# Performance work log

Hardware: AMD Instinct MI355X
Metric: run time of the kernel (lower is better)

The kernel has to match this reference:

```python
import jax, jax.numpy as jnp
import numpy as np

B, S, D = 1, 2048, 4096
H, KVH, HD = 32, 8, 128
ROPE_THETA = 10000.0


def setup_inputs() -> dict:
    key = jax.random.key(0)
    k1, k2, k3, k4, k5 = jax.random.split(key, 5)
    scale = D ** -0.5
    return {
        "hidden_states": jax.random.normal(k1, (B, S, D), dtype=jnp.float32),
        "position_ids": jnp.arange(S, dtype=jnp.int64).reshape(1, S),
        "Wq": jax.random.normal(k2, (H * HD, D), dtype=jnp.float32) * scale,
        "Wk": jax.random.normal(k3, (KVH * HD, D), dtype=jnp.float32) * scale,
        "Wv": jax.random.normal(k4, (KVH * HD, D), dtype=jnp.float32) * scale,
        "Wo": jax.random.normal(k5, (D, H * HD), dtype=jnp.float32) * scale,
    }


def _rotate_half(x):
    x1, x2 = x[..., : HD // 2], x[..., HD // 2 :]
    return jnp.concatenate((-x2, x1), axis=-1)


def reference(hidden_states, position_ids, Wq, Wk, Wv, Wo):
    b, s, d = hidden_states.shape
    # projections: nn.Linear applies x @ W.T
    q = jnp.einsum("bsd,ed->bse", hidden_states, Wq).reshape(b, s, H, HD).transpose(0, 2, 1, 3)
    k = jnp.einsum("bsd,ed->bse", hidden_states, Wk).reshape(b, s, KVH, HD).transpose(0, 2, 1, 3)
    v = jnp.einsum("bsd,ed->bse", hidden_states, Wv).reshape(b, s, KVH, HD).transpose(0, 2, 1, 3)
    # rotary embedding (default rope: inv_freq = theta^(-2i/d), attention_scaling = 1)
    inv_freq = 1.0 / (ROPE_THETA ** (jnp.arange(0, HD, 2, dtype=jnp.float32) / HD))
    pos = position_ids.astype(jnp.float32)  # [Bp, S]
    freqs = pos[:, :, None] * inv_freq[None, None, :]  # [Bp, S, HD/2]
    emb = jnp.concatenate((freqs, freqs), axis=-1)  # [Bp, S, HD]
    cos = jnp.cos(emb)[:, None, :, :]  # unsqueeze head dim
    sin = jnp.sin(emb)[:, None, :, :]
    q = q * cos + _rotate_half(q) * sin
    k = k * cos + _rotate_half(k) * sin
    # GQA: expand kv heads to match query heads
    groups = H // KVH
    k = jnp.repeat(k, groups, axis=1)
    v = jnp.repeat(v, groups, axis=1)
    # causal attention, scaling = head_dim^-0.5
    scores = jnp.einsum("bhqd,bhkd->bhqk", q, k) * (HD ** -0.5)
    causal = jnp.tril(jnp.ones((s, s), dtype=bool))
    scores = jnp.where(causal[None, None], scores, jnp.finfo(scores.dtype).min)
    attn = jax.nn.softmax(scores, axis=-1)
    out = jnp.einsum("bhqk,bhkd->bhqd", attn, v)
    out = out.transpose(0, 2, 1, 3).reshape(b, s, H * HD)
    return jnp.einsum("bse,de->bsd", out, Wo)
```

## Files before the change

### kernel.cpp

```cpp
#include <hip/hip_runtime.h>
#include <stdint.h>

typedef unsigned short u16;
typedef __attribute__((ext_vector_type(4))) float f32x4;
typedef __attribute__((ext_vector_type(8))) short bf16x8;

static constexpr int S   = 2048;
static constexpr int DM  = 4096;
static constexpr int NH  = 32;
static constexpr int NKV = 8;
static constexpr int HD  = 128;
static constexpr int LDQ = 5120;

__device__ __forceinline__ u16 f2bf(float f) {
    union { float f; unsigned u; } v; v.f = f;
    return (u16)((v.u + 0x7FFFu + ((v.u >> 16) & 1u)) >> 16);
}
__device__ __forceinline__ float bf2f(u16 h) {
    union { unsigned u; float f; } v; v.u = ((unsigned)h) << 16;
    return v.f;
}
__device__ __forceinline__ unsigned pk2bf(float lo, float hi) {
    unsigned r;
    asm("v_cvt_pk_bf16_f32 %0, %1, %2" : "=v"(r) : "v"(lo), "v"(hi));
    return r;
}

__device__ __forceinline__ void mfma16(f32x4& d, bf16x8 a, bf16x8 b) {
    asm("v_mfma_f32_16x16x32_bf16 %0, %1, %2, %0" : "+v"(d) : "v"(a), "v"(b));
}

__device__ __forceinline__ void gload_lds16(const u16* g, u16* lds) {
    __builtin_amdgcn_global_load_lds((__attribute__((address_space(1))) void*)g,
                                     (__attribute__((address_space(3))) void*)lds,
                                     16, 0, 0);
}

__global__ __launch_bounds__(256) void cvt_all(const float* __restrict__ X,
                                               const float* __restrict__ Wq,
                                               const float* __restrict__ Wk,
                                               const float* __restrict__ Wv,
                                               const float* __restrict__ Wo,
                                               u16* __restrict__ out) {
    const int n4 = 12582912;
    int i = blockIdx.x * blockDim.x + threadIdx.x;
    int stride = gridDim.x * blockDim.x;
    for (; i < n4; i += stride) {
        float4 v;
        if (i < 2097152)       v = ((const float4*)X)[i];
        else if (i < 6291456)  v = ((const float4*)Wq)[i - 2097152];
        else if (i < 7340032)  v = ((const float4*)Wk)[i - 6291456];
        else if (i < 8388608)  v = ((const float4*)Wv)[i - 7340032];
        else                   v = ((const float4*)Wo)[i - 8388608];
        ushort4 o;
        o.x = f2bf(v.x); o.y = f2bf(v.y); o.z = f2bf(v.z); o.w = f2bf(v.w);
        ((ushort4*)out)[i] = o;
    }
}

__global__ __launch_bounds__(256) void rope_table_kernel(float2* __restrict__ tbl) {
    int i = blockIdx.x * blockDim.x + threadIdx.x;
    if (i >= S * 64) return;
    int p = i >> 6, j = i & 63;
    float inv = powf(10000.0f, -(float)j / 64.0f);
    float a = (float)p * inv;
    tbl[i] = make_float2(cosf(a), sinf(a));
}

__global__ __launch_bounds__(256) void rope2_kernel(u16* __restrict__ X,
                                                    const float2* __restrict__ tbl,
                                                    float qscale) {
    int i = blockIdx.x * blockDim.x + threadIdx.x;
    const int total = S * 40 * 64;
    if (i >= total) return;
    int dd = i & 63;
    int t2 = i >> 6;
    int hh = t2 % 40;
    int s  = t2 / 40;
    size_t base;
    float scale;
    if (hh < 32) { base = (size_t)s * LDQ + hh * HD + dd;               scale = qscale; }
    else         { base = (size_t)s * LDQ + 4096 + (hh - 32) * HD + dd; scale = 1.0f;   }
    float x1 = bf2f(X[base]);
    float x2 = bf2f(X[base + 64]);
    float2 cs = tbl[(s << 6) + dd];
    X[base]      = f2bf((x1 * cs.x - x2 * cs.y) * scale);
    X[base + 64] = f2bf((x2 * cs.x + x1 * cs.y) * scale);
}

__global__ __launch_bounds__(256)
void gemm_bt(const u16* __restrict__ A, const u16* __restrict__ Bt,
             float* __restrict__ C, int M, int N, int K, int lda, int ldb, int ldc) {
    __shared__ u16 Al[128 * 64];
    __shared__ u16 Bl[128 * 64];
    const int t = threadIdx.x;
    const int w = t >> 6, l = t & 63;
    const int r16 = l & 15, g4 = l >> 4;
    const int m0 = blockIdx.y * 128, n0 = blockIdx.x * 128;
    const int wr = (w >> 1) * 64, wc = (w & 1) * 64;

    f32x4 acc[4][4];
#pragma unroll
    for (int i = 0; i < 4; ++i)
#pragma unroll
        for (int j = 0; j < 4; ++j) acc[i][j] = f32x4{0.f, 0.f, 0.f, 0.f};

    for (int kt = 0; kt < K; kt += 64) {
#pragma unroll
        for (int i = 0; i < 4; ++i) {
            int c = i * 256 + t;
            int r = c >> 3, s = (c & 7) ^ (r & 7);
            gload_lds16(A + (size_t)(m0 + r) * lda + kt + (s << 3),
                        Al + ((i * 256 + w * 64) << 3));
        }
#pragma unroll
        for (int i = 0; i < 4; ++i) {
            int c = i * 256 + t;
            int r = c >> 3, s = (c & 7) ^ (r & 7);
            gload_lds16(Bt + (size_t)(n0 + r) * ldb + kt + (s << 3),
                        Bl + ((i * 256 + w * 64) << 3));
        }
        asm volatile("s_waitcnt vmcnt(0)" ::: "memory");
        __syncthreads();

#pragma unroll
        for (int kk = 0; kk < 2; ++kk) {
            bf16x8 af[4], bfr[4];
#pragma unroll
            for (int mi = 0; mi < 4; ++mi) {
                int r = wr + mi * 16 + r16;
                af[mi] = *(const bf16x8*)((const char*)Al +
                          ((r * 128 + kk * 64 + g4 * 16) ^ ((r & 7) << 4)));
            }
#pragma unroll
            for (int ni = 0; ni < 4; ++ni) {
                int r = wc + ni * 16 + r16;
                bfr[ni] = *(const bf16x8*)((const char*)Bl +
                           ((r * 128 + kk * 64 + g4 * 16) ^ ((r & 7) << 4)));
            }
#pragma unroll
            for (int mi = 0; mi < 4; ++mi)
#pragma unroll
                for (int ni = 0; ni < 4; ++ni)
                    mfma16(acc[mi][ni], af[mi], bfr[ni]);
        }
        __syncthreads();
    }

    const int rb = g4 * 4;
#pragma unroll
    for (int mi = 0; mi < 4; ++mi)
#pragma unroll
        for (int ni = 0; ni < 4; ++ni) {
            const int n = n0 + wc + ni * 16 + r16;
            const int mbase = m0 + wr + mi * 16 + rb;
#pragma unroll
            for (int j = 0; j < 4; ++j)
                C[(size_t)(mbase + j) * ldc + n] = acc[mi][ni][j];
        }
}

__global__ __launch_bounds__(256)
void gemm_qkv(const u16* __restrict__ A, const u16* __restrict__ Bt,
              u16* __restrict__ Cqk, u16* __restrict__ Vt) {
    __shared__ u16 Al[128 * 64];
    __shared__ u16 Bl[128 * 64];
    const int t = threadIdx.x;
    const int w = t >> 6, l = t & 63;
    const int r16 = l & 15, g4 = l >> 4;
    const int m0 = blockIdx.y * 128, n0 = blockIdx.x * 128;
    const int wr = (w >> 1) * 64, wc = (w & 1) * 64;

    f32x4 acc[4][4];
#pragma unroll
    for (int i = 0; i < 4; ++i)
#pragma unroll
        for (int j = 0; j < 4; ++j) acc[i][j] = f32x4{0.f, 0.f, 0.f, 0.f};

    for (int kt = 0; kt < DM; kt += 64) {
#pragma unroll
        for (int i = 0; i < 4; ++i) {
            int c = i * 256 + t;
            int r = c >> 3, s = (c & 7) ^ (r & 7);
            gload_lds16(A + (size_t)(m0 + r) * DM + kt + (s << 3),
                        Al + ((i * 256 + w * 64) << 3));
        }
#pragma unroll
        for (int i = 0; i < 4; ++i) {
            int c = i * 256 + t;
            int r = c >> 3, s = (c & 7) ^ (r & 7);
            gload_lds16(Bt + (size_t)(n0 + r) * DM + kt + (s << 3),
                        Bl + ((i * 256 + w * 64) << 3));
        }
        asm volatile("s_waitcnt vmcnt(0)" ::: "memory");
        __syncthreads();

#pragma unroll
        for (int kk = 0; kk < 2; ++kk) {
            bf16x8 af[4], bfr[4];
#pragma unroll
            for (int mi = 0; mi < 4; ++mi) {
                int r = wr + mi * 16 + r16;
                af[mi] = *(const bf16x8*)((const char*)Al +
                          ((r * 128 + kk * 64 + g4 * 16) ^ ((r & 7) << 4)));
            }
#pragma unroll
            for (int ni = 0; ni < 4; ++ni) {
                int r = wc + ni * 16 + r16;
                bfr[ni] = *(const bf16x8*)((const char*)Bl +
                           ((r * 128 + kk * 64 + g4 * 16) ^ ((r & 7) << 4)));
            }
#pragma unroll
            for (int mi = 0; mi < 4; ++mi)
#pragma unroll
                for (int ni = 0; ni < 4; ++ni)
                    mfma16(acc[mi][ni], af[mi], bfr[ni]);
        }
        __syncthreads();
    }

    const int rb = g4 * 4;
    if (n0 < 5120) {
#pragma unroll
        for (int mi = 0; mi < 4; ++mi)
#pragma unroll
            for (int ni = 0; ni < 4; ++ni) {
                const int n = n0 + wc + ni * 16 + r16;
                const int mbase = m0 + wr + mi * 16 + rb;
#pragma unroll
                for (int j = 0; j < 4; ++j)
                    Cqk[(size_t)(mbase + j) * LDQ + n] = f2bf(acc[mi][ni][j]);
            }
    } else {
#pragma unroll
        for (int mi = 0; mi < 4; ++mi)
#pragma unroll
            for (int ni = 0; ni < 4; ++ni) {
                const int n = n0 + wc + ni * 16 + r16 - 5120;
                const int mbase = m0 + wr + mi * 16 + rb;
                ushort4 v4;
                v4.x = f2bf(acc[mi][ni][0]); v4.y = f2bf(acc[mi][ni][1]);
                v4.z = f2bf(acc[mi][ni][2]); v4.w = f2bf(acc[mi][ni][3]);
                *(ushort4*)&Vt[(size_t)n * S + mbase] = v4;
            }
    }
}

__global__ __launch_bounds__(256, 2)
void attn_fwd(const u16* __restrict__ QK, const u16* __restrict__ Vt,
              u16* __restrict__ O) {
    __shared__ u16 Kl[2][64 * 128];
    __shared__ u16 Vl[2][128 * 64];
    __shared__ u16 Pl[4 * 1024];

    const int t = threadIdx.x;
    const int w = t >> 6, l = t & 63;
    const int r16 = l & 15, g4 = l >> 4;
    const int h = blockIdx.y;
    const int kvh = h >> 2;
    const int p = blockIdx.x;
    const int q0A = p * 64, q0B = (31 - p) * 64;
    const int ntA = p + 1, ntB = 32 - p;

    const u16* Kg = QK + 4096 + kvh * HD;
    const u16* Vg = Vt + (size_t)(kvh * HD) * S;
    u16* Pb = &Pl[w * 1024];

    bf16x8 qfA[4], qfB[4];
    {
        const u16* Qg = QK + h * HD;
        const size_t qrA = (size_t)(q0A + w * 16 + r16) * LDQ;
        const size_t qrB = (size_t)(q0B + w * 16 + r16) * LDQ;
#pragma unroll
        for (int kg = 0; kg < 4; ++kg) {
            qfA[kg] = *(const bf16x8*)&Qg[qrA + kg * 32 + g4 * 8];
            qfB[kg] = *(const bf16x8*)&Qg[qrB + kg * 32 + g4 * 8];
        }
    }

    f32x4 accA[8], accB[8];
    float mA = -3.0e38f, lA = 0.f, mB = -3.0e38f, lB = 0.f;
#pragma unroll
    for (int i = 0; i < 8; ++i) { accA[i] = f32x4{0,0,0,0}; accB[i] = f32x4{0,0,0,0}; }

    auto stage = [&](int tk, int b) {
        const int kv0 = tk * 64;
#pragma unroll
        for (int i = 0; i < 4; ++i) {
            int c = i * 256 + t;
            int r = c >> 4, s = (c & 15) ^ (r & 7);
            gload_lds16(Kg + (size_t)(kv0 + r) * LDQ + (s << 3),
                        &Kl[b][0] + ((i * 256 + w * 64) << 3));
        }
#pragma unroll
        for (int i = 0; i < 4; ++i) {
            int c = i * 256 + t;
            int r = c >> 3, s = (c & 7) ^ (r & 7);
            gload_lds16(Vg + (size_t)r * S + kv0 + (s << 3),
                        &Vl[b][0] + ((i * 256 + w * 64) << 3));
        }
    };

    auto compute = [&](f32x4 (&acco)[8], float& mrun, float& lrun,
                       const bf16x8 (&qf)[4], int q0, int tk, bool maskit, int b) {
        const int kv0 = tk * 64;
        const u16* Kb = &Kl[b][0];
        const u16* Vb = &Vl[b][0];

        f32x4 sc[4];
#pragma unroll
        for (int ni = 0; ni < 4; ++ni) sc[ni] = f32x4{0,0,0,0};
        __builtin_amdgcn_s_setprio(1);
#pragma unroll
        for (int kg = 0; kg < 4; ++kg) {
#pragma unroll
            for (int ni = 0; ni < 4; ++ni) {
                int row = ni * 16 + r16;
                int bb = (row * 256 + kg * 64 + g4 * 16) ^ ((row & 7) << 4);
                bf16x8 kf = *(const bf16x8*)((const char*)Kb + bb);
                mfma16(sc[ni], kf, qf[kg]);
            }
        }
        __builtin_amdgcn_s_setprio(0);

        const int qg = q0 + (w << 4) + r16;
        if (maskit) {
#pragma unroll
            for (int ni = 0; ni < 4; ++ni)
#pragma unroll
                for (int j = 0; j < 4; ++j)
                    if (kv0 + ni * 16 + g4 * 4 + j > qg) sc[ni][j] = -3.0e38f;
        }

        float v = fmaxf(fmaxf(fmaxf(sc[0][0], sc[0][1]), fmaxf(sc[0][2], sc[0][3])),
                        fmaxf(fmaxf(sc[1][0], sc[1][1]), fmaxf(sc[1][2], sc[1][3])));
        v = fmaxf(v, fmaxf(fmaxf(fmaxf(sc[2][0], sc[2][1]), fmaxf(sc[2][2], sc[2][3])),
                           fmaxf(fmaxf(sc[3][0], sc[3][1]), fmaxf(sc[3][2], sc[3][3]))));
        v = fmaxf(v, __shfl_xor(v, 16));
        v = fmaxf(v, __shfl_xor(v, 32));

        float facl = 1.f;
        if (__any(v > mrun + 11.5f)) {
            float nm = fmaxf(mrun, v);
            facl = exp2f(mrun - nm);
            mrun = nm;
            float fj[4];
#pragma unroll
            for (int j = 0; j < 4; ++j) fj[j] = __shfl(facl, g4 * 4 + j, 16);
#pragma unroll
            for (int i = 0; i < 8; ++i)
#pragma unroll
                for (int j = 0; j < 4; ++j) acco[i][j] *= fj[j];
        }
#pragma unroll
        for (int ni = 0; ni < 4; ++ni)
#pragma unroll
            for (int j = 0; j < 4; ++j) sc[ni][j] = exp2f(sc[ni][j] - mrun);

        float s2 = ((sc[0][0] + sc[0][1]) + (sc[0][2] + sc[0][3]))
                 + ((sc[1][0] + sc[1][1]) + (sc[1][2] + sc[1][3]))
                 + ((sc[2][0] + sc[2][1]) + (sc[2][2] + sc[2][3]))
                 + ((sc[3][0] + sc[3][1]) + (sc[3][2] + sc[3][3]));
        s2 += __shfl_xor(s2, 16);
        s2 += __shfl_xor(s2, 32);
        lrun = lrun * facl + s2;

        {
            char* pp = (char*)Pb;
            const int swz = (r16 & 7) << 4;
            const int rowb = r16 * 128;
#pragma unroll
            for (int ti = 0; ti < 4; ++ti) {
                unsigned r01 = pk2bf(sc[ti][0], sc[ti][1]);
                unsigned r23 = pk2bf(sc[ti][2], sc[ti][3]);
                const int colb = (ti * 16 + g4 * 4) << 1;
                *(unsigned*)(pp + ((rowb + colb) ^ swz))     = r01;
                *(unsigned*)(pp + ((rowb + colb + 4) ^ swz)) = r23;
            }
        }
        asm volatile("s_waitcnt lgkmcnt(0)" ::: "memory");
        __builtin_amdgcn_sched_barrier(0);

        int pb0 = (r16 * 128 + g4 * 16) ^ ((r16 & 7) << 4);
        bf16x8 pf0 = *(const bf16x8*)((const char*)Pb + pb0);
        bf16x8 pf1 = *(const bf16x8*)((const char*)Pb + (pb0 ^ 64));
        __builtin_amdgcn_s_setprio(1);
#pragma unroll
        for (int ni = 0; ni < 8; ++ni) {
            int row = ni * 16 + r16;
            int bb = (row * 128 + g4 * 16) ^ ((row & 7) << 4);
            bf16x8 v0 = *(const bf16x8*)((const char*)Vb + bb);
            mfma16(acco[ni], pf0, v0);
            bf16x8 v1 = *(const bf16x8*)((const char*)Vb + (bb ^ 64));
            mfma16(acco[ni], pf1, v1);
        }
        __builtin_amdgcn_s_setprio(0);
    };

    auto epilogue = [&](f32x4 (&acco)[8], float lrun, int q0) {
        float rlr = 1.0f / lrun;
        float rl[4];
#pragma unroll
        for (int j = 0; j < 4; ++j) rl[j] = __shfl(rlr, g4 * 4 + j, 16);
#pragma unroll
        for (int ni = 0; ni < 8; ++ni)
#pragma unroll
            for (int j = 0; j < 4; ++j) {
                const int qg = q0 + w * 16 + g4 * 4 + j;
                O[(size_t)qg * DM + h * HD + ni * 16 + r16] = f2bf(acco[ni][j] * rl[j]);
            }
    };

    stage(0, 0);
    asm volatile("s_waitcnt vmcnt(0)" ::: "memory");
    __syncthreads();
    int buf = 0;

    for (int tk = 0; tk < ntB; ++tk) {
        if (tk + 1 < ntB) stage(tk + 1, buf ^ 1);
        compute(accB, mB, lB, qfB, q0B, tk, tk == ntB - 1, buf);
        if (tk < ntA) compute(accA, mA, lA, qfA, q0A, tk, tk == ntA - 1, buf);
        asm volatile("s_waitcnt vmcnt(0)" ::: "memory");
        __syncthreads();
        buf ^= 1;
    }
    epilogue(accA, lA, q0A);
    epilogue(accB, lB, q0B);
}

extern "C" void kernel_launch(void* const* d_in, const int* in_sizes, int n_in,
                              void* d_out, int out_size, void* d_ws, size_t ws_size,
                              hipStream_t stream) {
    const float* X  = (const float*)d_in[0];
    const float* Wq = (const float*)d_in[2];
    const float* Wk = (const float*)d_in[3];
    const float* Wv = (const float*)d_in[4];
    const float* Wo = (const float*)d_in[5];

    char* ws = (char*)d_ws;
    u16*    Xbf  = (u16*)(ws + 0);
    u16*    Wqkv = (u16*)(ws + 16777216);
    u16*    Wobf = (u16*)(ws + 67108864);
    u16*    QKb  = (u16*)(ws + 100663296);
    u16*    Vtbf = (u16*)(ws + 121634816);
    u16*    Obf  = (u16*)(ws + 125829120);
    float2* tbl  = (float2*)(ws + 142606336);
    if (ws_size < 143654912ull) return;

    dim3 blk(256);

    cvt_all<<<2048, blk, 0, stream>>>(X, Wq, Wk, Wv, Wo, (u16*)ws);
    rope_table_kernel<<<(S * 64 + 255) / 256, blk, 0, stream>>>(tbl);

    gemm_qkv<<<dim3(48, 16), blk, 0, stream>>>(Xbf, Wqkv, QKb, Vtbf);

    rope2_kernel<<<(S * 40 * 64 + 255) / 256, blk, 0, stream>>>(
        QKb, tbl, 0.08838834764831845f * 1.4426950408889634f);

    attn_fwd<<<dim3(16, NH), blk, 0, stream>>>(QKb, Vtbf, Obf);

    gemm_bt<<<dim3(DM / 128, S / 128), blk, 0, stream>>>(
        Obf, Wobf, (float*)d_out, S, DM, DM, DM, DM, DM);
}
```

Baseline: 339.2 us.

## Fuse paired Q-tile attention steps to share K/V LDS fragment loads

When both query tiles (A and B) process the same KV tile, the new compute_pair path loads each K and V fragment from LDS once and issues MFMAs for both tiles, with separate P buffers per tile. This halves LDS reads for K and V in the paired phase and interleaves independent MFMA chains for more instruction-level parallelism. It raises register pressure (two score sets and four P fragments live at once) and adds 8 KB of LDS, which may lower occupancy under launch_bounds(256,2).

```diff
diff --git a/kernel.cpp b/kernel.cpp
--- a/kernel.cpp
+++ b/kernel.cpp
@@ -251,7 +251,8 @@
               u16* __restrict__ O) {
     __shared__ u16 Kl[2][64 * 128];
     __shared__ u16 Vl[2][128 * 64];
-    __shared__ u16 Pl[4 * 1024];
+    __shared__ u16 PlB[4 * 1024];
+    __shared__ u16 PlA[4 * 1024];
 
     const int t = threadIdx.x;
     const int w = t >> 6, l = t & 63;
@@ -264,7 +265,8 @@
 
     const u16* Kg = QK + 4096 + kvh * HD;
     const u16* Vg = Vt + (size_t)(kvh * HD) * S;
-    u16* Pb = &Pl[w * 1024];
+    u16* PbB = &PlB[w * 1024];
+    u16* PbA = &PlA[w * 1024];
 
     bf16x8 qfA[4], qfB[4];
     {
@@ -301,28 +303,9 @@
         }
     };
 
-    auto compute = [&](f32x4 (&acco)[8], float& mrun, float& lrun,
-                       const bf16x8 (&qf)[4], int q0, int tk, bool maskit, int b) {
-        const int kv0 = tk * 64;
-        const u16* Kb = &Kl[b][0];
-        const u16* Vb = &Vl[b][0];
-
-        f32x4 sc[4];
-#pragma unroll
-        for (int ni = 0; ni < 4; ++ni) sc[ni] = f32x4{0,0,0,0};
-        __builtin_amdgcn_s_setprio(1);
-#pragma unroll
-        for (int kg = 0; kg < 4; ++kg) {
-#pragma unroll
-            for (int ni = 0; ni < 4; ++ni) {
-                int row = ni * 16 + r16;
-                int bb = (row * 256 + kg * 64 + g4 * 16) ^ ((row & 7) << 4);
-                bf16x8 kf = *(const bf16x8*)((const char*)Kb + bb);
-                mfma16(sc[ni], kf, qf[kg]);
-            }
-        }
-        __builtin_amdgcn_s_setprio(0);
-
+    auto softmax = [&](f32x4 (&sc)[4], float& mrun, float& lrun, f32x4 (&acco)[8],
+                       int q0, int kv0, bool maskit, u16* Pbuf,
+                       bf16x8& pf0, bf16x8& pf1) {
         const int qg = q0 + (w << 4) + r16;
         if (maskit) {
 #pragma unroll
@@ -366,7 +349,7 @@
         lrun = lrun * facl + s2;
 
         {
-            char* pp = (char*)Pb;
+            char* pp = (char*)Pbuf;
             const int swz = (r16 & 7) << 4;
             const int rowb = r16 * 128;
 #pragma unroll
@@ -382,17 +365,85 @@
         __builtin_amdgcn_sched_barrier(0);
 
         int pb0 = (r16 * 128 + g4 * 16) ^ ((r16 & 7) << 4);
-        bf16x8 pf0 = *(const bf16x8*)((const char*)Pb + pb0);
-        bf16x8 pf1 = *(const bf16x8*)((const char*)Pb + (pb0 ^ 64));
+        pf0 = *(const bf16x8*)((const char*)Pbuf + pb0);
+        pf1 = *(const bf16x8*)((const char*)Pbuf + (pb0 ^ 64));
+        __builtin_amdgcn_sched_barrier(0);
+    };
+
+    auto compute_single = [&](int tk, int b, bool maskit) {
+        const int kv0 = tk * 64;
+        const u16* Kb = &Kl[b][0];
+        const u16* Vb = &Vl[b][0];
+
+        f32x4 sc[4];
+#pragma unroll
+        for (int ni = 0; ni < 4; ++ni) sc[ni] = f32x4{0,0,0,0};
+        __builtin_amdgcn_s_setprio(1);
+#pragma unroll
+        for (int kg = 0; kg < 4; ++kg) {
+#pragma unroll
+            for (int ni = 0; ni < 4; ++ni) {
+                int row = ni * 16 + r16;
+                int bb = (row * 256 + kg * 64 + g4 * 16) ^ ((row & 7) << 4);
+                bf16x8 kf = *(const bf16x8*)((const char*)Kb + bb);
+                mfma16(sc[ni], kf, qfB[kg]);
+            }
+        }
+        __builtin_amdgcn_s_setprio(0);
+
+        bf16x8 pf0, pf1;
+        softmax(sc, mB, lB, accB, q0B, kv0, maskit, PbB, pf0, pf1);
+
         __builtin_amdgcn_s_setprio(1);
 #pragma unroll
         for (int ni = 0; ni < 8; ++ni) {
             int row = ni * 16 + r16;
             int bb = (row * 128 + g4 * 16) ^ ((row & 7) << 4);
             bf16x8 v0 = *(const bf16x8*)((const char*)Vb + bb);
-            mfma16(acco[ni], pf0, v0);
+            mfma16(accB[ni], pf0, v0);
             bf16x8 v1 = *(const bf16x8*)((const char*)Vb + (bb ^ 64));
-            mfma16(acco[ni], pf1, v1);
+            mfma16(accB[ni], pf1, v1);
+        }
+        __builtin_amdgcn_s_setprio(0);
+    };
+
+    auto compute_pair = [&](int tk, int b, bool maskA, bool maskB) {
+        const int kv0 = tk * 64;
+        const u16* Kb = &Kl[b][0];
+        const u16* Vb = &Vl[b][0];
+
+        f32x4 scA[4], scB[4];
+#pragma unroll
+        for (int ni = 0; ni < 4; ++ni) { scA[ni] = f32x4{0,0,0,0}; scB[ni] = f32x4{0,0,0,0}; }
+        __builtin_amdgcn_s_setprio(1);
+#pragma unroll
+        for (int kg = 0; kg < 4; ++kg) {
+#pragma unroll
+            for (int ni = 0; ni < 4; ++ni) {
+                int row = ni * 16 + r16;
+                int bb = (row * 256 + kg * 64 + g4 * 16) ^ ((row & 7) << 4);
+                bf16x8 kf = *(const bf16x8*)((const char*)Kb + bb);
+                mfma16(scB[ni], kf, qfB[kg]);
+                mfma16(scA[ni], kf, qfA[kg]);
+            }
+        }
+        __builtin_amdgcn_s_setprio(0);
+
+        bf16x8 pfB0, pfB1, pfA0, pfA1;
+        softmax(scB, mB, lB, accB, q0B, kv0, maskB, PbB, pfB0, pfB1);
+        softmax(scA, mA, lA, accA, q0A, kv0, maskA, PbA, pfA0, pfA1);
+
+        __builtin_amdgcn_s_setprio(1);
+#pragma unroll
+        for (int ni = 0; ni < 8; ++ni) {
+            int row = ni * 16 + r16;
+            int bb = (row * 128 + g4 * 16) ^ ((row & 7) << 4);
+            bf16x8 v0 = *(const bf16x8*)((const char*)Vb + bb);
+            bf16x8 v1 = *(const bf16x8*)((const char*)Vb + (bb ^ 64));
+            mfma16(accB[ni], pfB0, v0);
+            mfma16(accB[ni], pfB1, v1);
+            mfma16(accA[ni], pfA0, v0);
+            mfma16(accA[ni], pfA1, v1);
         }
         __builtin_amdgcn_s_setprio(0);
     };
@@ -418,8 +469,8 @@
 
     for (int tk = 0; tk < ntB; ++tk) {
         if (tk + 1 < ntB) stage(tk + 1, buf ^ 1);
-        compute(accB, mB, lB, qfB, q0B, tk, tk == ntB - 1, buf);
-        if (tk < ntA) compute(accA, mA, lA, qfA, q0A, tk, tk == ntA - 1, buf);
+        if (tk < ntA) compute_pair(tk, buf, tk == ntA - 1, tk == ntB - 1);
+        else          compute_single(tk, buf, tk == ntB - 1);
         asm volatile("s_waitcnt vmcnt(0)" ::: "memory");
         __syncthreads();
         buf ^= 1;
```

Measured after the change: 404.4 us. +19.2%, slower.
